# Performance work log

Hardware: AMD Instinct MI355X
Metric: run time of the kernel (lower is better)

## Reference

```python
import jax, jax.numpy as jnp
import numpy as np

N, M = 50000, 12
A, NBR = 128, 64  # atom_fea_len, nbr_fea_len
EPS = 1e-5


def setup_inputs() -> dict:
    key = jax.random.key(0)
    ks = jax.random.split(key, 6)
    atom_in_fea = jax.random.normal(ks[0], (N, A), dtype=jnp.float32)
    nbr_fea = jax.random.normal(ks[1], (N, M, NBR), dtype=jnp.float32)
    nbr_fea_idx = jax.random.randint(ks[2], (N, M), 0, N)
    tabulated_padding_fillter = jax.random.randint(ks[3], (N, M), 0, 2).astype(jnp.float32)
    fan_in = 2 * A + NBR
    W_fc = jax.random.normal(ks[4], (fan_in, 2 * A), dtype=jnp.float32) * (1.0 / np.sqrt(fan_in))
    b_fc = jnp.zeros((2 * A,), dtype=jnp.float32)
    gamma1 = jnp.ones((2 * A,), dtype=jnp.float32)
    beta1 = jnp.zeros((2 * A,), dtype=jnp.float32)
    gamma2 = jnp.ones((A,), dtype=jnp.float32)
    beta2 = jnp.zeros((A,), dtype=jnp.float32)
    return dict(atom_in_fea=atom_in_fea, nbr_fea=nbr_fea, nbr_fea_idx=nbr_fea_idx,
                tabulated_padding_fillter=tabulated_padding_fillter,
                W_fc=W_fc, b_fc=b_fc, gamma1=gamma1, beta1=beta1,
                gamma2=gamma2, beta2=beta2)


def reference(atom_in_fea, nbr_fea, nbr_fea_idx, tabulated_padding_fillter,
              W_fc, b_fc, gamma1, beta1, gamma2, beta2):
    n, m = nbr_fea_idx.shape
    a = atom_in_fea.shape[1]
    # gather neighbor atom features: (N, M, A)
    atom_nbr_fea = atom_in_fea[nbr_fea_idx]
    self_fea = jnp.broadcast_to(atom_in_fea[:, None, :], (n, m, a))
    total_nbr_fea = jnp.concatenate([self_fea, atom_nbr_fea, nbr_fea], axis=2)  # (N, M, 2A+NBR)
    total_gated_fea = total_nbr_fea @ W_fc + b_fc  # (N, M, 2A)

    # masked BatchNorm (training mode): stats over rows where filter == 1
    flat = total_gated_fea.reshape(-1, 2 * a)  # (N*M, 2A)
    mask = tabulated_padding_fillter.reshape(-1)  # (N*M,)
    cnt = jnp.sum(mask)
    mw = mask[:, None]
    mean1 = jnp.sum(flat * mw, axis=0) / cnt
    var1 = jnp.sum(((flat - mean1) ** 2) * mw, axis=0) / cnt  # biased, as torch BN
    normed = (flat - mean1) * jax.lax.rsqrt(var1 + EPS) * gamma1 + beta1
    flat = jnp.where(mw == 1, normed, flat)  # only masked rows replaced
    total_gated_fea = flat.reshape(n, m, 2 * a)

    nbr_filter, nbr_core = jnp.split(total_gated_fea, 2, axis=2)
    nbr_sumed = jnp.sum(jax.nn.sigmoid(nbr_filter) * jax.nn.softplus(nbr_core)
                        * tabulated_padding_fillter[:, :, None], axis=1)  # (N, A)

    # BatchNorm over all N rows (training-mode batch stats)
    mean2 = jnp.mean(nbr_sumed, axis=0)
    var2 = jnp.var(nbr_sumed, axis=0)
    nbr_sumed = (nbr_sumed - mean2) * jax.lax.rsqrt(var2 + EPS) * gamma2 + beta2

    return jax.nn.softplus(atom_in_fea + nbr_sumed)
```

## Files before the change

kernel.cpp:

```cpp
#include <hip/hip_runtime.h>

typedef unsigned short u16;
typedef unsigned int u32;

#define N_ATOM   50000
#define M_NBR    12
#define A_FEA    128
#define NBR_FEA  64
#define KDIM     320
#define CDIM     256
#define ROWS     600000
#define RPB      48
#define NBLK     12500
#define KC       10
#define EPSV     1e-5f
#define A_PITCH  656
#define GRID1    256
#define BUFSZ    31744
#define MASK_OFF 31488

using frag  = __attribute__((ext_vector_type(8))) short;
using f32x4 = __attribute__((ext_vector_type(4))) float;

#define WS_SUM1      0
#define WS_SUMSQ1    256
#define WS_CNT       512
#define WS_SUM2      516
#define WS_SUMSQ2    644
#define WS_STATS_END 772
#define WS_SCALE1    1024
#define WS_SHIFT1    1280
#define WS_SCALE2    1536
#define WS_SHIFT2    1664
#define WS_NBR       2048
#define WS_W_FOFF    (2048 + 6400000)
#define WS_P_FOFF    (2048 + 6400000 + 40960)
#define WS_G_FOFF    (WS_P_FOFF + 6400000)
#define WS_NEED_BYTES 358572032ull

__device__ __forceinline__ u32 fbits(float f) { union { float f; u32 u; } v; v.f = f; return v.u; }
__device__ __forceinline__ float bits2f(u32 u) { union { u32 u; float f; } v; v.u = u; return v.f; }
__device__ __forceinline__ u32 pkbf(float a, float b) {
    return __builtin_amdgcn_perm(fbits(b) + 0x8000u, fbits(a) + 0x8000u, 0x07060302u);
}
__device__ __forceinline__ u16 f2bf1(float f) { return (u16)((fbits(f) + 0x8000u) >> 16); }
__device__ __forceinline__ float bf2f(u16 u) { return bits2f(((u32)u) << 16); }
__device__ __forceinline__ float softplusf(float x) {
    return fmaxf(x, 0.f) + __logf(1.f + __expf(-fabsf(x)));
}
__device__ __forceinline__ float sigmoidf(float x) {
    return __builtin_amdgcn_rcpf(1.f + __expf(-x));
}

__global__ void swizzleW(const float* __restrict__ W, u16* __restrict__ wsW) {
    int g = blockIdx.x * 256 + threadIdx.x;
    if (g >= KDIM * CDIM) return;
    int k = g >> 8, n = g & 255;
    u32 u = fbits(W[g]);
    u32 r = u + 0x7fffu + ((u >> 16) & 1u);
    wsW[((k >> 5) * 256 + n) * 32 + (k & 31)] = (u16)(r >> 16);
}

__global__ __launch_bounds__(256) void mask_cnt(const float* __restrict__ mask, float* __restrict__ ws) {
    int t = blockIdx.x * 256 + threadIdx.x;
    float s = 0.f;
    if (t < 37500) {
        const float* p = mask + (size_t)t * 16;
        #pragma unroll
        for (int i = 0; i < 4; i++) {
            float4 v = *(const float4*)(p + i * 4);
            s += (v.x + v.y) + (v.z + v.w);
        }
    }
    #pragma unroll
    for (int d = 1; d < 64; d <<= 1) s += __shfl_xor(s, d, 64);
    __shared__ float r[4];
    int l = threadIdx.x & 63, w = threadIdx.x >> 6;
    if (l == 0) r[w] = s;
    __syncthreads();
    if (threadIdx.x == 0) atomicAdd(&ws[WS_CNT], r[0] + r[1] + r[2] + r[3]);
}

struct Meta {
    int   idx[3];
    float mg[3];
    float mnA, mnB;
    float mrow;
};
struct Data {
    float4 sv, gv[3], nva, nvb;
};

__device__ __forceinline__ void load_meta(Meta& M, const int* __restrict__ nbridx,
                                          const float* __restrict__ mask,
                                          int r0, int w, int l, int tid) {
    const int h32 = l >> 5;
    #pragma unroll
    for (int j = 0; j < 3; ++j) {
        int row = 6 * w + 2 * j + h32;
        M.idx[j] = nbridx[r0 + row];
        M.mg[j]  = mask[r0 + row];
    }
    M.mnA = mask[r0 + 6 * w + (l >> 4)];
    M.mnB = (l < 32) ? mask[r0 + 6 * w + 4 + (l >> 4)] : 0.f;
    M.mrow = (tid < 48) ? mask[r0 + tid] : 0.f;
}

__device__ __forceinline__ void load_data(Data& D, const Meta& M,
                                          const float* __restrict__ atom,
                                          const float* __restrict__ nbrf,
                                          int t, int w, int l) {
    const int c32 = l & 31;
    D.sv = *(const float4*)(atom + (size_t)(t * 4 + (w >> 1)) * 128 + c32 * 4);
    #pragma unroll
    for (int j = 0; j < 3; ++j)
        if (M.mg[j] != 0.f)
            D.gv[j] = *(const float4*)(atom + (size_t)M.idx[j] * 128 + c32 * 4);
    const float* nb = nbrf + (size_t)(t * RPB + 6 * w) * 64;
    if (M.mnA != 0.f) D.nva = *(const float4*)(nb + (l >> 4) * 64 + (l & 15) * 4);
    if (l < 32 && M.mnB != 0.f) D.nvb = *(const float4*)(nb + (4 + (l >> 4)) * 64 + (l & 15) * 4);
}

__device__ __forceinline__ void write_tile(const Data& D, const Meta& M, char* nb,
                                           int w, int l, int tid) {
    const int h32 = l >> 5, c32 = l & 31;
    {
        uint2 p; p.x = pkbf(D.sv.x, D.sv.y); p.y = pkbf(D.sv.z, D.sv.w);
        #pragma unroll
        for (int jj = 0; jj < 3; ++jj)
            *(uint2*)(nb + (6 * w + 3 * h32 + jj) * A_PITCH + c32 * 8) = p;
    }
    #pragma unroll
    for (int j = 0; j < 3; ++j) {
        int row = 6 * w + 2 * j + h32;
        uint2 g; g.x = 0u; g.y = 0u;
        if (M.mg[j] != 0.f) { g.x = pkbf(D.gv[j].x, D.gv[j].y); g.y = pkbf(D.gv[j].z, D.gv[j].w); }
        *(uint2*)(nb + row * A_PITCH + 256 + c32 * 8) = g;
    }
    {
        int rowA = 6 * w + (l >> 4);
        uint2 na; na.x = 0u; na.y = 0u;
        if (M.mnA != 0.f) { na.x = pkbf(D.nva.x, D.nva.y); na.y = pkbf(D.nva.z, D.nva.w); }
        *(uint2*)(nb + rowA * A_PITCH + 512 + (l & 15) * 8) = na;
    }
    if (l < 32) {
        int rowB = 6 * w + 4 + (l >> 4);
        uint2 nv; nv.x = 0u; nv.y = 0u;
        if (M.mnB != 0.f) { nv.x = pkbf(D.nvb.x, D.nvb.y); nv.y = pkbf(D.nvb.z, D.nvb.w); }
        *(uint2*)(nb + rowB * A_PITCH + 512 + (l & 15) * 8) = nv;
    }
    if (tid < 48) *(float*)(nb + MASK_OFF + tid * 4) = M.mrow;
}

__global__ __launch_bounds__(512, 2) void gemm1_pipe(
    const float* __restrict__ atom, const float* __restrict__ nbrf,
    const int* __restrict__ nbridx, const float* __restrict__ mask,
    const u16* __restrict__ wsW, float* __restrict__ ws)
{
    __shared__ __align__(16) char smem[2 * BUFSZ];
    const int tid = threadIdx.x;
    const int w = tid >> 6, l = tid & 63, l15 = l & 15, l4 = l >> 4;
    float* __restrict__ P = ws + WS_P_FOFF;
    u32* __restrict__ Hbase = (u32*)(ws + WS_G_FOFF);

    frag Bf[KC][2];
    #pragma unroll
    for (int kk = 0; kk < KC; ++kk)
        #pragma unroll
        for (int cf = 0; cf < 2; ++cf)
            Bf[kk][cf] = *(const frag*)((const char*)wsW +
                ((size_t)(kk * 256 + cf * 128 + 16 * w + l15) * 64 + l4 * 16));

    Meta M; Data D;
    const int t0 = blockIdx.x;

    load_meta(M, nbridx, mask, t0 * RPB, w, l, tid);
    load_data(D, M, atom, nbrf, t0, w, l);
    write_tile(D, M, smem, w, l, tid);
    if (t0 + GRID1 < NBLK)
        load_meta(M, nbridx, mask, (t0 + GRID1) * RPB, w, l, tid);
    __syncthreads();

    int cur = 0;
    for (int t = t0; t < NBLK; t += GRID1) {
        const int tn = t + GRID1;
        const bool hasNext = (tn < NBLK);
        char* bufc = smem + cur * BUFSZ;
        char* bufn = smem + (cur ^ 1) * BUFSZ;

        if (hasNext) load_data(D, M, atom, nbrf, tn, w, l);

        f32x4 acc[3][2];
        #pragma unroll
        for (int rf = 0; rf < 3; ++rf) {
            acc[rf][0] = (f32x4){0.f, 0.f, 0.f, 0.f};
            acc[rf][1] = (f32x4){0.f, 0.f, 0.f, 0.f};
        }
        const char* Ac = bufc + l15 * A_PITCH + l4 * 16;
        #pragma unroll
        for (int kk = 0; kk < KC; ++kk) {
            frag a[3];
            #pragma unroll
            for (int rf = 0; rf < 3; ++rf)
                a[rf] = *(const frag*)(Ac + rf * 16 * A_PITCH + kk * 64);
            #pragma unroll
            for (int rf = 0; rf < 3; ++rf) {
                acc[rf][0] = __builtin_amdgcn_mfma_f32_16x16x32_bf16(a[rf], Bf[kk][0], acc[rf][0], 0, 0, 0);
                acc[rf][1] = __builtin_amdgcn_mfma_f32_16x16x32_bf16(a[rf], Bf[kk][1], acc[rf][1], 0, 0, 0);
            }
        }

        f32x4 mm[3];
        #pragma unroll
        for (int rf = 0; rf < 3; ++rf)
            mm[rf] = *(const f32x4*)(bufc + MASK_OFF + (rf * 16 + l4 * 4) * 4);
        #pragma unroll
        for (int cf = 0; cf < 2; ++cf) {
            float s = 0.f, q = 0.f;
            #pragma unroll
            for (int rf = 0; rf < 3; ++rf)
                #pragma unroll
                for (int rg = 0; rg < 4; ++rg) {
                    float mv = mm[rf][rg];
                    float v = acc[rf][cf][rg];
                    s += mv * v; q += mv * v * v;
                }
            s += __shfl_xor(s, 16, 64); s += __shfl_xor(s, 32, 64);
            q += __shfl_xor(q, 16, 64); q += __shfl_xor(q, 32, 64);
            if (l4 == 0) {
                int col = cf * 128 + 16 * w + l15;
                P[(size_t)t * 512 + col]       = s;
                P[(size_t)t * 512 + 256 + col] = q;
            }
        }
        {
            u32* H = Hbase + (size_t)t * (RPB * 128) + 16 * w + l15;
            #pragma unroll
            for (int rf = 0; rf < 3; ++rf)
                #pragma unroll
                for (int rg = 0; rg < 4; ++rg) {
                    const int row = rf * 16 + l4 * 4 + rg;
                    if (mm[rf][rg] != 0.f)
                        H[(size_t)row * 128] = pkbf(acc[rf][0][rg], acc[rf][1][rg]);
                }
        }

        if (hasNext) write_tile(D, M, bufn, w, l, tid);
        if (tn + GRID1 < NBLK)
            load_meta(M, nbridx, mask, (tn + GRID1) * RPB, w, l, tid);
        __syncthreads();
        cur ^= 1;
    }
}

template <int MODE>
__global__ __launch_bounds__(256, 3) void gemm_pass(
    const float* __restrict__ atom, const float* __restrict__ nbrf,
    const int* __restrict__ nbridx, const float* __restrict__ mask,
    const u16* __restrict__ wsW, float* __restrict__ ws)
{
    __shared__ __align__(16) char smem[RPB * A_PITCH];
    __shared__ float m_lds[RPB];
    __shared__ int   idx_lds[RPB];
    __shared__ float red[(MODE == 2) ? 4 : 1][128];

    const int tid = threadIdx.x;
    const int w = tid >> 6, l = tid & 63, l15 = l & 15, l4 = l >> 4;
    const int h32 = l >> 5, c32 = l & 31;
    const int blk = blockIdx.x;
    const int r0 = blk * RPB;
    float* __restrict__ P = ws + WS_P_FOFF;

    if (tid < RPB) {
        m_lds[tid] = mask[r0 + tid];
        idx_lds[tid] = nbridx[r0 + tid];
    }
    __syncthreads();

    {
        float4 sv = *(const float4*)(atom + (size_t)(blk * 4 + w) * 128 + c32 * 4);
        uint2 p; p.x = pkbf(sv.x, sv.y); p.y = pkbf(sv.z, sv.w);
        #pragma unroll
        for (int jj = 0; jj < 6; ++jj) {
            int row = 12 * w + 6 * h32 + jj;
            *(uint2*)(smem + row * A_PITCH + c32 * 8) = p;
        }
    }
    {
        float4 v[6]; float mrow[6];
        #pragma unroll
        for (int i = 0; i < 6; ++i) {
            int row = 12 * w + 2 * i + h32;
            mrow[i] = m_lds[row];
            if (mrow[i] != 0.f)
                v[i] = *(const float4*)(atom + (size_t)idx_lds[row] * 128 + c32 * 4);
        }
        #pragma unroll
        for (int i = 0; i < 6; ++i) {
            int row = 12 * w + 2 * i + h32;
            uint2 p; p.x = 0u; p.y = 0u;
            if (mrow[i] != 0.f) { p.x = pkbf(v[i].x, v[i].y); p.y = pkbf(v[i].z, v[i].w); }
            *(uint2*)(smem + row * A_PITCH + 256 + c32 * 8) = p;
        }
    }
    {
        const float* nf = nbrf + (size_t)(r0 + 12 * w) * 64;
        float4 v[3]; float mrow[3]; int rowv[3], cv[3];
        #pragma unroll
        for (int i = 0; i < 3; ++i) {
            int g = i * 64 + l;
            rowv[i] = 12 * w + (g >> 4);
            cv[i] = g & 15;
            mrow[i] = m_lds[rowv[i]];
            if (mrow[i] != 0.f) v[i] = *(const float4*)(nf + g * 4);
        }
        #pragma unroll
        for (int i = 0; i < 3; ++i) {
            uint2 p; p.x = 0u; p.y = 0u;
            if (mrow[i] != 0.f) { p.x = pkbf(v[i].x, v[i].y); p.y = pkbf(v[i].z, v[i].w); }
            *(uint2*)(smem + rowv[i] * A_PITCH + 512 + cv[i] * 8) = p;
        }
    }
    __syncthreads();

    f32x4 acc[3][4];
    #pragma unroll
    for (int rf = 0; rf < 3; rf++)
        #pragma unroll
        for (int cf = 0; cf < 4; cf++)
            acc[rf][cf] = (f32x4){0.f, 0.f, 0.f, 0.f};

    const char* Ab = smem + l15 * A_PITCH + l4 * 16;
    const char* Bb = (const char*)wsW + ((size_t)w * 2048 + l15 * 64 + l4 * 16);
    frag bcur[4], bnext[4];
    #pragma unroll
    for (int cf = 0; cf < 4; ++cf)
        bcur[cf] = *(const frag*)(Bb + cf * 1024 + (cf >= 2 ? 6144 : 0));
    #pragma unroll
    for (int kk = 0; kk < KC; ++kk) {
        if (kk < KC - 1) {
            const char* Bn = Bb + (kk + 1) * 16384;
            #pragma unroll
            for (int cf = 0; cf < 4; ++cf)
                bnext[cf] = *(const frag*)(Bn + cf * 1024 + (cf >= 2 ? 6144 : 0));
        }
        frag a[3];
        #pragma unroll
        for (int rf = 0; rf < 3; rf++)
            a[rf] = *(const frag*)(Ab + rf * 16 * A_PITCH + kk * 64);
        #pragma unroll
        for (int rf = 0; rf < 3; rf++)
            #pragma unroll
            for (int cf = 0; cf < 4; cf++)
                acc[rf][cf] = __builtin_amdgcn_mfma_f32_16x16x32_bf16(a[rf], bcur[cf], acc[rf][cf], 0, 0, 0);
        #pragma unroll
        for (int cf = 0; cf < 4; ++cf) bcur[cf] = bnext[cf];
    }

    if constexpr (MODE == 0) {
        #pragma unroll
        for (int cf = 0; cf < 4; cf++) {
            float s = 0.f, q = 0.f;
            #pragma unroll
            for (int rf = 0; rf < 3; rf++)
                #pragma unroll
                for (int rg = 0; rg < 4; rg++) {
                    int row = rf * 16 + l4 * 4 + rg;
                    float mv = m_lds[row];
                    float v = acc[rf][cf][rg];
                    s += mv * v; q += mv * v * v;
                }
            s += __shfl_xor(s, 16, 64); s += __shfl_xor(s, 32, 64);
            q += __shfl_xor(q, 16, 64); q += __shfl_xor(q, 32, 64);
            if (l4 == 0) {
                int col = w * 32 + cf * 16 + (cf >= 2 ? 96 : 0) + l15;
                P[(size_t)blk * 512 + col]       = s;
                P[(size_t)blk * 512 + 256 + col] = q;
            }
        }
    } else {
        __syncthreads();
        u16* g16 = (u16*)smem;
        #pragma unroll
        for (int cf = 0; cf < 4; cf++) {
            int col = w * 32 + cf * 16 + (cf >= 2 ? 96 : 0) + l15;
            float sc = ws[WS_SCALE1 + col];
            float sh = ws[WS_SHIFT1 + col];
            #pragma unroll
            for (int rf = 0; rf < 3; rf++)
                #pragma unroll
                for (int rg = 0; rg < 4; rg++) {
                    int row = rf * 16 + l4 * 4 + rg;
                    g16[row * 256 + col] = f2bf1(acc[rf][cf][rg] * sc + sh);
                }
        }
        __syncthreads();
        int h = tid >> 7;
        int c = tid & 127;
        float ns0 = 0.f, ns1 = 0.f;
        #pragma unroll
        for (int la2 = 0; la2 < 2; la2++) {
            int la = h * 2 + la2;
            float a_ns = 0.f;
            #pragma unroll
            for (int j = 0; j < 12; j++) {
                int row = la * 12 + j;
                float f = bf2f(g16[row * 256 + c]);
                float k = bf2f(g16[row * 256 + 128 + c]);
                a_ns += m_lds[row] * sigmoidf(f) * softplusf(k);
            }
            ws[WS_NBR + (blk * 4 + la) * 128 + c] = a_ns;
            if (la2 == 0) ns0 = a_ns; else ns1 = a_ns;
        }
        red[h][c]     = ns0 + ns1;
        red[2 + h][c] = ns0 * ns0 + ns1 * ns1;
        __syncthreads();
        if (tid < 128) {
            P[(size_t)blk * 256 + tid]       = red[0][tid] + red[1][tid];
            P[(size_t)blk * 256 + 128 + tid] = red[2][tid] + red[3][tid];
        }
    }
}

__global__ __launch_bounds__(256) void pass2_gate(
    const float* __restrict__ ws_ro, const float* __restrict__ mask, float* __restrict__ ws)
{
    __shared__ float m_lds[RPB];
    __shared__ float red[4][128];

    const int tid = threadIdx.x;
    const int blk = blockIdx.x;
    const int h = tid >> 7, c = tid & 127;
    float* __restrict__ P = ws + WS_P_FOFF;

    if (tid < RPB) m_lds[tid] = mask[blk * RPB + tid];
    __syncthreads();

    const float scf = ws_ro[WS_SCALE1 + c],       shf = ws_ro[WS_SHIFT1 + c];
    const float sck = ws_ro[WS_SCALE1 + 128 + c], shk = ws_ro[WS_SHIFT1 + 128 + c];

    const u32* Hb = (const u32*)(ws_ro + WS_G_FOFF) + (size_t)blk * (RPB * 128) + c;

    float ns0 = 0.f, ns1 = 0.f;
    #pragma unroll
    for (int la2 = 0; la2 < 2; la2++) {
        const int la = h * 2 + la2;
        u32 v[12]; float mv[12];
        #pragma unroll
        for (int j = 0; j < 12; j++) {
            mv[j] = m_lds[la * 12 + j];
            if (mv[j] != 0.f) v[j] = Hb[(size_t)(la * 12 + j) * 128];
        }
        float a_ns = 0.f;
        #pragma unroll
        for (int j = 0; j < 12; j++) {
            if (mv[j] != 0.f) {
                const u32 u = v[j];
                float f = bits2f(u << 16)         * scf + shf;
                float k = bits2f(u & 0xffff0000u) * sck + shk;
                float sg = __builtin_amdgcn_rcpf(1.f + __expf(-f));
                float sp = fmaxf(k, 0.f) + __logf(1.f + __expf(-fabsf(k)));
                a_ns += sg * sp;
            }
        }
        ws[WS_NBR + (blk * 4 + la) * 128 + c] = a_ns;
        if (la2 == 0) ns0 = a_ns; else ns1 = a_ns;
    }
    red[h][c]     = ns0 + ns1;
    red[2 + h][c] = ns0 * ns0 + ns1 * ns1;
    __syncthreads();
    if (tid < 128) {
        P[(size_t)blk * 256 + tid]       = red[0][tid] + red[1][tid];
        P[(size_t)blk * 256 + 128 + tid] = red[2][tid] + red[3][tid];
    }
}

__global__ __launch_bounds__(256) void red1(const float* __restrict__ ws_ro, float* __restrict__ ws) {
    const float* P = ws_ro + WS_P_FOFF;
    int c = (blockIdx.x & 1) * 256 + threadIdx.x;
    int s = blockIdx.x >> 1;
    const float* p = P + (size_t)s * 100 * 512 + c;
    float a = 0.f;
    #pragma unroll 4
    for (int r = 0; r < 100; r++) a += p[(size_t)r * 512];
    atomicAdd(&ws[WS_SUM1 + c], a);
}

__global__ __launch_bounds__(256) void red2(const float* __restrict__ ws_ro, float* __restrict__ ws) {
    const float* P = ws_ro + WS_P_FOFF;
    int s = blockIdx.x;
    const float* p = P + (size_t)s * 100 * 256 + threadIdx.x;
    float a = 0.f;
    #pragma unroll 4
    for (int r = 0; r < 100; r++) a += p[(size_t)r * 256];
    atomicAdd(&ws[WS_SUM2 + threadIdx.x], a);
}

__global__ void finalize1(float* __restrict__ ws, const float* __restrict__ g1, const float* __restrict__ b1) {
    int c = threadIdx.x;
    float cnt = ws[WS_CNT];
    float mean = ws[WS_SUM1 + c] / cnt;
    float var  = ws[WS_SUMSQ1 + c] / cnt - mean * mean;
    float sc = g1[c] * rsqrtf(var + EPSV);
    ws[WS_SCALE1 + c] = sc;
    ws[WS_SHIFT1 + c] = b1[c] - mean * sc;
}

__global__ void finalize2(float* __restrict__ ws, const float* __restrict__ g2, const float* __restrict__ b2) {
    int c = threadIdx.x;
    float inv = 1.f / (float)N_ATOM;
    float mean = ws[WS_SUM2 + c] * inv;
    float var  = ws[WS_SUMSQ2 + c] * inv - mean * mean;
    float sc = g2[c] * rsqrtf(var + EPSV);
    ws[WS_SCALE2 + c] = sc;
    ws[WS_SHIFT2 + c] = b2[c] - mean * sc;
}

__global__ __launch_bounds__(256) void out_kernel(
    const float* __restrict__ atom, const float* __restrict__ ws, float* __restrict__ out)
{
    int g = blockIdx.x * 256 + threadIdx.x;
    if (g >= N_ATOM * 32) return;
    int i = g >> 5, c4 = (g & 31) * 4;
    float4 av = *(const float4*)(atom + i * 128 + c4);
    float4 nv = *(const float4*)(ws + WS_NBR + i * 128 + c4);
    float4 sc = *(const float4*)(ws + WS_SCALE2 + c4);
    float4 sh = *(const float4*)(ws + WS_SHIFT2 + c4);
    float4 ov;
    ov.x = softplusf(av.x + nv.x * sc.x + sh.x);
    ov.y = softplusf(av.y + nv.y * sc.y + sh.y);
    ov.z = softplusf(av.z + nv.z * sc.z + sh.z);
    ov.w = softplusf(av.w + nv.w * sc.w + sh.w);
    *(float4*)(out + i * 128 + c4) = ov;
}

extern "C" void kernel_launch(void* const* d_in, const int* in_sizes, int n_in,
                              void* d_out, int out_size, void* d_ws, size_t ws_size,
                              hipStream_t stream) {
    (void)in_sizes; (void)n_in; (void)out_size;
    const float* atom = (const float*)d_in[0];
    const float* nbrf = (const float*)d_in[1];
    const int*   nidx = (const int*)d_in[2];
    const float* mask = (const float*)d_in[3];
    const float* W    = (const float*)d_in[4];
    const float* g1 = (const float*)d_in[6];
    const float* b1 = (const float*)d_in[7];
    const float* g2 = (const float*)d_in[8];
    const float* b2 = (const float*)d_in[9];
    float* ws  = (float*)d_ws;
    u16*  wsW  = (u16*)((char*)d_ws + (size_t)WS_W_FOFF * 4);
    float* out = (float*)d_out;
    const bool bigws = (ws_size >= WS_NEED_BYTES);

    hipMemsetAsync(d_ws, 0, WS_STATS_END * 4, stream);
    swizzleW<<<(KDIM * CDIM + 255) / 256, 256, 0, stream>>>(W, wsW);
    mask_cnt<<<147, 256, 0, stream>>>(mask, ws);
    if (bigws) {
        gemm1_pipe<<<GRID1, 512, 0, stream>>>(atom, nbrf, nidx, mask, wsW, ws);
        red1<<<250, 256, 0, stream>>>(ws, ws);
        finalize1<<<1, 256, 0, stream>>>(ws, g1, b1);
        pass2_gate<<<NBLK, 256, 0, stream>>>(ws, mask, ws);
    } else {
        gemm_pass<0><<<NBLK, 256, 0, stream>>>(atom, nbrf, nidx, mask, wsW, ws);
        red1<<<250, 256, 0, stream>>>(ws, ws);
        finalize1<<<1, 256, 0, stream>>>(ws, g1, b1);
        gemm_pass<2><<<NBLK, 256, 0, stream>>>(atom, nbrf, nidx, mask, wsW, ws);
    }
    red2<<<125, 256, 0, stream>>>(ws, ws);
    finalize2<<<1, 128, 0, stream>>>(ws, g2, b2);
    out_kernel<<<(N_ATOM * 32 + 255) / 256, 256, 0, stream>>>(atom, ws, out);
}
```

Before: 462.4 us.

## Fold BN stat reductions into producer kernels via atomics, drop reduce/finalize launches

The pipelined GEMM now accumulates per-column sums, sums of squares and the mask count in registers across its persistent tiles, then adds them with atomics at the end, replacing the per-tile partial buffer, the mask_cnt kernel, red1 and finalize1. pass2_gate recomputes the BN1 scale and shift from the sums and atomically accumulates the BN2 sums. out_kernel derives the BN2 scale and shift inline, so red2 and finalize2 are removed on the fast path. This cuts several small launches and the partial-buffer traffic. In exchange it adds 12500 blocks of atomics on 256 addresses in pass2_gate and redundant per-thread stat math. Float atomics also make the summation order nondeterministic.

```diff
diff --git a/kernel.cpp b/kernel.cpp
--- a/kernel.cpp
+++ b/kernel.cpp
@@ -30,8 +30,6 @@
 #define WS_STATS_END 772
 #define WS_SCALE1    1024
 #define WS_SHIFT1    1280
-#define WS_SCALE2    1536
-#define WS_SHIFT2    1664
 #define WS_NBR       2048
 #define WS_W_FOFF    (2048 + 6400000)
 #define WS_P_FOFF    (2048 + 6400000 + 40960)
@@ -160,7 +158,6 @@
     __shared__ __align__(16) char smem[2 * BUFSZ];
     const int tid = threadIdx.x;
     const int w = tid >> 6, l = tid & 63, l15 = l & 15, l4 = l >> 4;
-    float* __restrict__ P = ws + WS_P_FOFF;
     u32* __restrict__ Hbase = (u32*)(ws + WS_G_FOFF);
 
     frag Bf[KC][2];
@@ -172,13 +169,18 @@
                 ((size_t)(kk * 256 + cf * 128 + 16 * w + l15) * 64 + l4 * 16));
 
     Meta M; Data D;
+    float cnt_acc = 0.f;
+    float sacc[2] = {0.f, 0.f}, qacc[2] = {0.f, 0.f};
     const int t0 = blockIdx.x;
 
     load_meta(M, nbridx, mask, t0 * RPB, w, l, tid);
+    cnt_acc += M.mrow;
     load_data(D, M, atom, nbrf, t0, w, l);
     write_tile(D, M, smem, w, l, tid);
-    if (t0 + GRID1 < NBLK)
+    if (t0 + GRID1 < NBLK) {
         load_meta(M, nbridx, mask, (t0 + GRID1) * RPB, w, l, tid);
+        cnt_acc += M.mrow;
+    }
     __syncthreads();
 
     int cur = 0;
@@ -227,11 +229,8 @@
                 }
             s += __shfl_xor(s, 16, 64); s += __shfl_xor(s, 32, 64);
             q += __shfl_xor(q, 16, 64); q += __shfl_xor(q, 32, 64);
-            if (l4 == 0) {
-                int col = cf * 128 + 16 * w + l15;
-                P[(size_t)t * 512 + col]       = s;
-                P[(size_t)t * 512 + 256 + col] = q;
-            }
+            sacc[cf] += s;
+            qacc[cf] += q;
         }
         {
             u32* H = Hbase + (size_t)t * (RPB * 128) + 16 * w + l15;
@@ -246,10 +245,27 @@
         }
 
         if (hasNext) write_tile(D, M, bufn, w, l, tid);
-        if (tn + GRID1 < NBLK)
+        if (tn + GRID1 < NBLK) {
             load_meta(M, nbridx, mask, (tn + GRID1) * RPB, w, l, tid);
+            cnt_acc += M.mrow;
+        }
         __syncthreads();
         cur ^= 1;
+    }
+
+    if (l4 == 0) {
+        #pragma unroll
+        for (int cf = 0; cf < 2; ++cf) {
+            int col = cf * 128 + 16 * w + l15;
+            atomicAdd(&ws[WS_SUM1 + col],   sacc[cf]);
+            atomicAdd(&ws[WS_SUMSQ1 + col], qacc[cf]);
+        }
+    }
+    if (w == 0) {
+        float c = cnt_acc;
+        #pragma unroll
+        for (int d = 1; d < 64; d <<= 1) c += __shfl_xor(c, d, 64);
+        if (l == 0) atomicAdd(&ws[WS_CNT], c);
     }
 }
 
@@ -423,7 +439,9 @@
 }
 
 __global__ __launch_bounds__(256) void pass2_gate(
-    const float* __restrict__ ws_ro, const float* __restrict__ mask, float* __restrict__ ws)
+    const float* __restrict__ ws_ro, const float* __restrict__ mask,
+    const float* __restrict__ g1, const float* __restrict__ b1,
+    float* __restrict__ ws)
 {
     __shared__ float m_lds[RPB];
     __shared__ float red[4][128];
@@ -431,13 +449,19 @@
     const int tid = threadIdx.x;
     const int blk = blockIdx.x;
     const int h = tid >> 7, c = tid & 127;
-    float* __restrict__ P = ws + WS_P_FOFF;
 
     if (tid < RPB) m_lds[tid] = mask[blk * RPB + tid];
+
+    const float rc = 1.f / ws_ro[WS_CNT];
+    float mf = ws_ro[WS_SUM1 + c] * rc;
+    float vf = ws_ro[WS_SUMSQ1 + c] * rc - mf * mf;
+    const float scf = g1[c] * rsqrtf(vf + EPSV);
+    const float shf = b1[c] - mf * scf;
+    float mk = ws_ro[WS_SUM1 + 128 + c] * rc;
+    float vk = ws_ro[WS_SUMSQ1 + 128 + c] * rc - mk * mk;
+    const float sck = g1[128 + c] * rsqrtf(vk + EPSV);
+    const float shk = b1[128 + c] - mk * sck;
     __syncthreads();
-
-    const float scf = ws_ro[WS_SCALE1 + c],       shf = ws_ro[WS_SHIFT1 + c];
-    const float sck = ws_ro[WS_SCALE1 + 128 + c], shk = ws_ro[WS_SHIFT1 + 128 + c];
 
     const u32* Hb = (const u32*)(ws_ro + WS_G_FOFF) + (size_t)blk * (RPB * 128) + c;
 
@@ -470,8 +494,8 @@
     red[2 + h][c] = ns0 * ns0 + ns1 * ns1;
     __syncthreads();
     if (tid < 128) {
-        P[(size_t)blk * 256 + tid]       = red[0][tid] + red[1][tid];
-        P[(size_t)blk * 256 + 128 + tid] = red[2][tid] + red[3][tid];
+        atomicAdd(&ws[WS_SUM2 + tid],   red[0][tid] + red[1][tid]);
+        atomicAdd(&ws[WS_SUMSQ2 + tid], red[2][tid] + red[3][tid]);
     }
 }
 
@@ -506,26 +530,26 @@
     ws[WS_SHIFT1 + c] = b1[c] - mean * sc;
 }
 
-__global__ void finalize2(float* __restrict__ ws, const float* __restrict__ g2, const float* __restrict__ b2) {
-    int c = threadIdx.x;
-    float inv = 1.f / (float)N_ATOM;
-    float mean = ws[WS_SUM2 + c] * inv;
-    float var  = ws[WS_SUMSQ2 + c] * inv - mean * mean;
-    float sc = g2[c] * rsqrtf(var + EPSV);
-    ws[WS_SCALE2 + c] = sc;
-    ws[WS_SHIFT2 + c] = b2[c] - mean * sc;
-}
-
 __global__ __launch_bounds__(256) void out_kernel(
-    const float* __restrict__ atom, const float* __restrict__ ws, float* __restrict__ out)
+    const float* __restrict__ atom, const float* __restrict__ ws,
+    const float* __restrict__ g2, const float* __restrict__ b2,
+    float* __restrict__ out)
 {
     int g = blockIdx.x * 256 + threadIdx.x;
     if (g >= N_ATOM * 32) return;
     int i = g >> 5, c4 = (g & 31) * 4;
+    const float inv = 1.f / (float)N_ATOM;
+    float4 s2  = *(const float4*)(ws + WS_SUM2 + c4);
+    float4 q2  = *(const float4*)(ws + WS_SUMSQ2 + c4);
+    float4 g2v = *(const float4*)(g2 + c4);
+    float4 b2v = *(const float4*)(b2 + c4);
+    float4 sc, sh;
+    { float m = s2.x * inv; sc.x = g2v.x * rsqrtf(q2.x * inv - m * m + EPSV); sh.x = b2v.x - m * sc.x; }
+    { float m = s2.y * inv; sc.y = g2v.y * rsqrtf(q2.y * inv - m * m + EPSV); sh.y = b2v.y - m * sc.y; }
+    { float m = s2.z * inv; sc.z = g2v.z * rsqrtf(q2.z * inv - m * m + EPSV); sh.z = b2v.z - m * sc.z; }
+    { float m = s2.w * inv; sc.w = g2v.w * rsqrtf(q2.w * inv - m * m + EPSV); sh.w = b2v.w - m * sc.w; }
     float4 av = *(const float4*)(atom + i * 128 + c4);
     float4 nv = *(const float4*)(ws + WS_NBR + i * 128 + c4);
-    float4 sc = *(const float4*)(ws + WS_SCALE2 + c4);
-    float4 sh = *(const float4*)(ws + WS_SHIFT2 + c4);
     float4 ov;
     ov.x = softplusf(av.x + nv.x * sc.x + sh.x);
     ov.y = softplusf(av.y + nv.y * sc.y + sh.y);
@@ -554,19 +578,16 @@
 
     hipMemsetAsync(d_ws, 0, WS_STATS_END * 4, stream);
     swizzleW<<<(KDIM * CDIM + 255) / 256, 256, 0, stream>>>(W, wsW);
-    mask_cnt<<<147, 256, 0, stream>>>(mask, ws);
     if (bigws) {
         gemm1_pipe<<<GRID1, 512, 0, stream>>>(atom, nbrf, nidx, mask, wsW, ws);
-        red1<<<250, 256, 0, stream>>>(ws, ws);
-        finalize1<<<1, 256, 0, stream>>>(ws, g1, b1);
-        pass2_gate<<<NBLK, 256, 0, stream>>>(ws, mask, ws);
+        pass2_gate<<<NBLK, 256, 0, stream>>>(ws, mask, g1, b1, ws);
     } else {
+        mask_cnt<<<147, 256, 0, stream>>>(mask, ws);
         gemm_pass<0><<<NBLK, 256, 0, stream>>>(atom, nbrf, nidx, mask, wsW, ws);
         red1<<<250, 256, 0, stream>>>(ws, ws);
         finalize1<<<1, 256, 0, stream>>>(ws, g1, b1);
         gemm_pass<2><<<NBLK, 256, 0, stream>>>(atom, nbrf, nidx, mask, wsW, ws);
-    }
-    red2<<<125, 256, 0, stream>>>(ws, ws);
-    finalize2<<<1, 128, 0, stream>>>(ws, g2, b2);
-    out_kernel<<<(N_ATOM * 32 + 255) / 256, 256, 0, stream>>>(atom, ws, out);
-}
+        red2<<<125, 256, 0, stream>>>(ws, ws);
+    }
+    out_kernel<<<(N_ATOM * 32 + 255) / 256, 256, 0, stream>>>(atom, ws, g2, b2, out);
+}
```

New measurement: 762.5 us. 64.9% more time.
